# Kernel optimization log

Measured on AMD Instinct MI355X. Metric: run time of the kernel, lower is better.

Reference implementation:

```python
import jax, jax.numpy as jnp
import numpy as np

B, S, E, H = 2, 2048, 1024, 16
DH = E // H


def setup_inputs() -> dict:
    key = jax.random.key(0)
    ks = jax.random.split(key, 12)
    std = 1.0 / np.sqrt(E)
    inp = {
        "query": jax.random.normal(ks[0], (B, S, E), jnp.float32),
        "key": jax.random.normal(ks[1], (B, S, E), jnp.float32),
        "value": jax.random.normal(ks[2], (B, S, E), jnp.float32),
        "mask": jax.random.randint(ks[3], (B, 1, 1, S), 0, 2, jnp.int32),
        "Wq": jax.random.normal(ks[4], (E, E), jnp.float32) * std,
        "bq": jnp.zeros((E,), jnp.float32),
        "Wk": jax.random.normal(ks[5], (E, E), jnp.float32) * std,
        "bk": jnp.zeros((E,), jnp.float32),
        "Wv": jax.random.normal(ks[6], (E, E), jnp.float32) * std,
        "bv": jnp.zeros((E,), jnp.float32),
        "Wo": jax.random.normal(ks[7], (E, E), jnp.float32) * std,
        "bo": jnp.zeros((E,), jnp.float32),
    }
    return inp


def reference(query, key, value, mask, Wq, bq, Wk, bk, Wv, bv, Wo, bo):
    b = query.shape[0]
    # QKV projections, then split heads: [B,S,E] -> [B,H,S,Dh]
    def split_heads(x):
        return x.reshape(b, -1, H, DH).transpose(0, 2, 1, 3)
    q = split_heads(query @ Wq + bq)
    k = split_heads(key @ Wk + bk)
    v = split_heads(value @ Wv + bv)
    # explicit bmm -> mask -> softmax -> bmm (non-SDPA), scores [B,H,Sq,Sk]
    scores = jnp.einsum("bhqd,bhkd->bhqk", q, k) / np.sqrt(DH).astype(np.float32)
    scores = jnp.where(mask == 0, jnp.float32(-1e9), scores)
    attn = jax.nn.softmax(scores, axis=-1)  # dropout is identity in eval mode
    out = jnp.einsum("bhqk,bhkd->bhqd", attn, v)
    out = out.transpose(0, 2, 1, 3).reshape(b, -1, E)  # merge heads
    return out @ Wo + bo
```

## Files before the change

### kernel.cpp

```cpp
#include <hip/hip_runtime.h>
#include <hip/hip_bf16.h>
#include <stdint.h>

#define B_ 2
#define S_ 2048
#define E_ 1024
#define H_ 16
#define DH_ 64
#define MELEMS (4096 * 1024)
#define WE (1024 * 1024)

typedef unsigned short u16;
typedef __bf16 bf16x8 __attribute__((ext_vector_type(8)));
typedef u16 u16x8 __attribute__((ext_vector_type(8)));
typedef u16 u16x4 __attribute__((ext_vector_type(4)));
typedef float f32x4 __attribute__((ext_vector_type(4)));
typedef uint32_t u32x4 __attribute__((ext_vector_type(4)));

__device__ __forceinline__ float bf2f(u16 u) {
    union { uint32_t i; float f; } v; v.i = ((uint32_t)u) << 16; return v.f;
}
__device__ __forceinline__ u16 f2bf(float f) {
    union { float f; uint32_t i; } v; v.f = f;
    uint32_t r = (v.i + 0x7FFFu + ((v.i >> 16) & 1u)) >> 16;
    return (u16)r;
}
__device__ __forceinline__ uint32_t pkbf(float a, float b) {
    __hip_bfloat162 h = __float22bfloat162_rn(make_float2(a, b));
    uint32_t r; __builtin_memcpy(&r, &h, 4);
    return r;
}
__device__ __forceinline__ bf16x8 ldfrag(const u16* p) {
    u16x8 t = *(const u16x8*)p;
    return __builtin_bit_cast(bf16x8, t);
}
__device__ __forceinline__ void gld16(const void* g, void* l) {
    __builtin_amdgcn_global_load_lds(
        (const __attribute__((address_space(1))) void*)g,
        (__attribute__((address_space(3))) void*)l, 16, 0, 0);
}

__global__ __launch_bounds__(256)
void cvt_all(const float* __restrict__ q, const float* __restrict__ k,
             const float* __restrict__ v,
             const float* __restrict__ W0, const float* __restrict__ W1,
             const float* __restrict__ W2, const float* __restrict__ W3,
             u16* __restrict__ Qi, u16* __restrict__ Ki, u16* __restrict__ Vi,
             u16* __restrict__ T0, u16* __restrict__ T1,
             u16* __restrict__ T2, u16* __restrict__ T3)
{
    __shared__ float tile[64][65];
    const int bid = blockIdx.x;
    const int tid = threadIdx.x;

    if (bid < 6144) {
        const int z = bid >> 11;
        const int cx = bid & 2047;
        const float* src = (z == 0) ? q : (z == 1) ? k : v;
        u16* dst = (z == 0) ? Qi : (z == 1) ? Ki : Vi;
        const size_t i8 = ((size_t)cx * 256 + tid) * 8;
        float4 f0 = *(const float4*)&src[i8];
        float4 f1 = *(const float4*)&src[i8 + 4];
        u16x8 t;
        t[0] = f2bf(f0.x); t[1] = f2bf(f0.y); t[2] = f2bf(f0.z); t[3] = f2bf(f0.w);
        t[4] = f2bf(f1.x); t[5] = f2bf(f1.y); t[6] = f2bf(f1.z); t[7] = f2bf(f1.w);
        *(u16x8*)&dst[i8] = t;
    } else {
        const int rr = bid - 6144;
        const int z = rr >> 8;
        const int tt = rr & 255;
        const float* W = (z == 0) ? W0 : (z == 1) ? W1 : (z == 2) ? W2 : W3;
        u16* T = (z == 0) ? T0 : (z == 1) ? T1 : (z == 2) ? T2 : T3;
        const int n0 = (tt & 15) * 64, k0 = (tt >> 4) * 64;
        const int r = tid >> 2, c0 = (tid & 3) * 16;

        #pragma unroll
        for (int i = 0; i < 4; ++i) {
            float4 w = *(const float4*)&W[(size_t)(k0 + r) * 1024 + n0 + c0 + i * 4];
            tile[r][c0 + i * 4 + 0] = w.x; tile[r][c0 + i * 4 + 1] = w.y;
            tile[r][c0 + i * 4 + 2] = w.z; tile[r][c0 + i * 4 + 3] = w.w;
        }
        __syncthreads();
        u16x8 a, b;
        #pragma unroll
        for (int j = 0; j < 8; ++j) a[j] = f2bf(tile[c0 + j][r]);
        #pragma unroll
        for (int j = 0; j < 8; ++j) b[j] = f2bf(tile[c0 + 8 + j][r]);
        *(u16x8*)&T[(size_t)(n0 + r) * 1024 + k0 + c0] = a;
        *(u16x8*)&T[(size_t)(n0 + r) * 1024 + k0 + c0 + 8] = b;
    }
}

template<int BN>
__global__ __launch_bounds__(256)
void gemm_bt(const u16* __restrict__ A0, const u16* __restrict__ A1,
             const u16* __restrict__ A2,
             const u16* __restrict__ Bt0, const u16* __restrict__ Bt1,
             const u16* __restrict__ Bt2,
             const float* __restrict__ b0, const float* __restrict__ b1,
             const float* __restrict__ b2,
             void* __restrict__ C0, void* __restrict__ C1, void* __restrict__ C2,
             int c_f32, int vt_z, float scale0, int K)
{
    const int z = blockIdx.z;
    const u16* A  = (z == 0) ? A0 : (z == 1) ? A1 : A2;
    const u16* Bt = (z == 0) ? Bt0 : (z == 1) ? Bt1 : Bt2;
    const float* bias = (z == 0) ? b0 : (z == 1) ? b1 : b2;
    void* C = (z == 0) ? C0 : (z == 1) ? C1 : C2;
    const float scale = (z == 0) ? scale0 : 1.0f;

    __shared__ alignas(16) u16 As[128 * 32];
    __shared__ alignas(16) u16 Bs[BN * 32];

    const int tid  = threadIdx.x;
    const int lane = tid & 63;
    const int wv   = tid >> 6;
    const int l15  = lane & 15;
    const int quad = lane >> 4;
    const int m0 = blockIdx.y * 128;
    const int n0 = blockIdx.x * BN;
    const int wr = (wv >> 1) * 64;
    const int wc = (wv & 1) * (BN / 2);

    const int srow = wv * 16 + (lane >> 2);
    const int skk  = (lane & 3) * 8;

    constexpr int NJ = BN / 32;
    f32x4 acc[4][NJ] = {};

    for (int k0 = 0; k0 < K; k0 += 32) {
        __syncthreads();
        #pragma unroll
        for (int h = 0; h < 2; ++h) {
            const int r = h * 64 + srow;
            gld16(&A[(size_t)(m0 + r) * K + k0 + skk], &As[r * 32 + skk]);
        }
        #pragma unroll
        for (int h = 0; h < BN / 64; ++h) {
            const int r = h * 64 + srow;
            gld16(&Bt[(size_t)(n0 + r) * K + k0 + skk], &Bs[r * 32 + skk]);
        }
        __syncthreads();

        bf16x8 a[4], b[NJ];
        #pragma unroll
        for (int i = 0; i < 4; ++i)
            a[i] = ldfrag(&As[(wr + i * 16 + l15) * 32 + quad * 8]);
        #pragma unroll
        for (int j = 0; j < NJ; ++j)
            b[j] = ldfrag(&Bs[(wc + j * 16 + l15) * 32 + quad * 8]);
        #pragma unroll
        for (int i = 0; i < 4; ++i)
            #pragma unroll
            for (int j = 0; j < NJ; ++j)
                acc[i][j] = __builtin_amdgcn_mfma_f32_16x16x32_bf16(
                    a[i], b[j], acc[i][j], 0, 0, 0);
    }

    #pragma unroll
    for (int j = 0; j < NJ; ++j) {
        const int col = n0 + wc + j * 16 + l15;
        const float bcol = bias[col];
        #pragma unroll
        for (int i = 0; i < 4; ++i) {
            if (z == vt_z) {
                const int row0 = m0 + wr + i * 16 + quad * 4;
                const int bb = row0 >> 11, s0 = row0 & 2047;
                u16x4 t;
                #pragma unroll
                for (int r = 0; r < 4; ++r) t[r] = f2bf((acc[i][j][r] + bcol) * scale);
                *(u16x4*)&((u16*)C)[((size_t)bb * E_ + col) * S_ + s0] = t;
            } else {
                #pragma unroll
                for (int r = 0; r < 4; ++r) {
                    const int row = m0 + wr + i * 16 + quad * 4 + r;
                    const float v = (acc[i][j][r] + bcol) * scale;
                    if (c_f32) ((float*)C)[(size_t)row * 1024 + col] = v;
                    else       ((u16*)C)[(size_t)row * 1024 + col]  = f2bf(v);
                }
            }
        }
    }
}

__global__ __launch_bounds__(256, 2)
void attn_v5(const u16* __restrict__ Q, const u16* __restrict__ K,
             const u16* __restrict__ Vt_g, const int* __restrict__ mask,
             u16* __restrict__ ctx)
{
    __shared__ alignas(16) u16 Ks[2][64 * 64];
    __shared__ alignas(16) u16 Vs[2][64 * 64];
    __shared__ alignas(16) float Sb[4][32 * 68];

    const int tid  = threadIdx.x;
    const int lane = tid & 63;
    const int wv   = tid >> 6;
    const int l15  = lane & 15;
    const int quad = lane >> 4;
    const int sw   = l15 & 7;
    const int qt = blockIdx.x;
    const int bh = blockIdx.y;
    const int b  = bh >> 4, h = bh & 15;

    const size_t qk_off = (size_t)b * S_ * E_ + (size_t)h * DH_;
    const size_t vt_off = ((size_t)b * E_ + (size_t)h * DH_) * S_;

    const int qr0 = qt * 128 + wv * 16 + l15;
    const int qr1 = qr0 + 64;
    const bf16x8 qa0 = ldfrag(&Q[qk_off + (size_t)qr0 * E_ + quad * 8]);
    const bf16x8 qa1 = ldfrag(&Q[qk_off + (size_t)qr0 * E_ + 32 + quad * 8]);
    const bf16x8 qb0 = ldfrag(&Q[qk_off + (size_t)qr1 * E_ + quad * 8]);
    const bf16x8 qb1 = ldfrag(&Q[qk_off + (size_t)qr1 * E_ + 32 + quad * 8]);

    u16x8 ou;
    #pragma unroll
    for (int j = 0; j < 8; ++j) ou[j] = 0x3F80;
    const bf16x8 ones = __builtin_bit_cast(bf16x8, ou);

    f32x4 oacc[2][4] = {};
    f32x4 lacc[2] = {};

    const int srow = tid >> 3;
    const int sp   = tid & 7;
    const int sg   = sp ^ (srow & 7);

    auto stage = [&](int kc, int buf) {
        #pragma unroll
        for (int g = 0; g < 2; ++g) {
            const int r = g * 32 + srow;
            gld16(&K[qk_off + (size_t)(kc + r) * E_ + sg * 8],
                  &Ks[buf][r * 64 + sp * 8]);
            gld16(&Vt_g[vt_off + (size_t)r * S_ + kc + sg * 8],
                  &Vs[buf][r * 64 + sp * 8]);
        }
    };

    stage(0, 0);
    int cur = 0;

    for (int kc = 0; kc < S_; kc += 64) {
        __syncthreads();
        if (kc + 64 < S_) stage(kc + 64, cur ^ 1);

        #pragma unroll
        for (int t = 0; t < 4; ++t) {
            const int R = t * 16 + l15;
            bf16x8 kf0 = ldfrag(&Ks[cur][R * 64 + (quad ^ sw) * 8]);
            bf16x8 kf1 = ldfrag(&Ks[cur][R * 64 + ((4 + quad) ^ sw) * 8]);
            f32x4 s0 = {}, s1 = {};
            s0 = __builtin_amdgcn_mfma_f32_16x16x32_bf16(qa0, kf0, s0, 0, 0, 0);
            s0 = __builtin_amdgcn_mfma_f32_16x16x32_bf16(qa1, kf1, s0, 0, 0, 0);
            s1 = __builtin_amdgcn_mfma_f32_16x16x32_bf16(qb0, kf0, s1, 0, 0, 0);
            s1 = __builtin_amdgcn_mfma_f32_16x16x32_bf16(qb1, kf1, s1, 0, 0, 0);
            const int mv = mask[b * S_ + kc + t * 16 + l15];
            #pragma unroll
            for (int r = 0; r < 4; ++r) {
                Sb[wv][(quad * 4 + r) * 68 + t * 16 + l15]      = mv ? s0[r] : -1e9f;
                Sb[wv][(16 + quad * 4 + r) * 68 + t * 16 + l15] = mv ? s1[r] : -1e9f;
            }
        }

        bf16x8 pa[2][2];
        #pragma unroll
        for (int s = 0; s < 2; ++s) {
            const float* row = &Sb[wv][(s * 16 + l15) * 68];
            f32x4 s0a = *(const f32x4*)&row[quad * 8];
            f32x4 s0b = *(const f32x4*)&row[quad * 8 + 4];
            f32x4 s1a = *(const f32x4*)&row[32 + quad * 8];
            f32x4 s1b = *(const f32x4*)&row[32 + quad * 8 + 4];
            u32x4 w0, w1;
            w0[0] = pkbf(__expf(s0a[0]), __expf(s0a[1]));
            w0[1] = pkbf(__expf(s0a[2]), __expf(s0a[3]));
            w0[2] = pkbf(__expf(s0b[0]), __expf(s0b[1]));
            w0[3] = pkbf(__expf(s0b[2]), __expf(s0b[3]));
            w1[0] = pkbf(__expf(s1a[0]), __expf(s1a[1]));
            w1[1] = pkbf(__expf(s1a[2]), __expf(s1a[3]));
            w1[2] = pkbf(__expf(s1b[0]), __expf(s1b[1]));
            w1[3] = pkbf(__expf(s1b[2]), __expf(s1b[3]));
            pa[s][0] = __builtin_bit_cast(bf16x8, w0);
            pa[s][1] = __builtin_bit_cast(bf16x8, w1);
        }

        #pragma unroll
        for (int c = 0; c < 4; ++c) {
            const int D = c * 16 + l15;
            bf16x8 vb0 = ldfrag(&Vs[cur][D * 64 + (quad ^ sw) * 8]);
            bf16x8 vb1 = ldfrag(&Vs[cur][D * 64 + ((4 + quad) ^ sw) * 8]);
            #pragma unroll
            for (int s = 0; s < 2; ++s) {
                oacc[s][c] = __builtin_amdgcn_mfma_f32_16x16x32_bf16(pa[s][0], vb0, oacc[s][c], 0, 0, 0);
                oacc[s][c] = __builtin_amdgcn_mfma_f32_16x16x32_bf16(pa[s][1], vb1, oacc[s][c], 0, 0, 0);
            }
        }
        #pragma unroll
        for (int s = 0; s < 2; ++s) {
            lacc[s] = __builtin_amdgcn_mfma_f32_16x16x32_bf16(pa[s][0], ones, lacc[s], 0, 0, 0);
            lacc[s] = __builtin_amdgcn_mfma_f32_16x16x32_bf16(pa[s][1], ones, lacc[s], 0, 0, 0);
        }
        cur ^= 1;
    }

    #pragma unroll
    for (int s = 0; s < 2; ++s)
        #pragma unroll
        for (int c = 0; c < 4; ++c) {
            const int e = h * DH_ + c * 16 + l15;
            #pragma unroll
            for (int r = 0; r < 4; ++r) {
                const int qg = qt * 128 + s * 64 + wv * 16 + quad * 4 + r;
                ctx[((size_t)b * S_ + qg) * E_ + e] = f2bf(oacc[s][c][r] / lacc[s][r]);
            }
        }
}

__global__ __launch_bounds__(256)
void gemm_bias(const void* __restrict__ A, int a_f32,
               const float* __restrict__ W, const float* __restrict__ bias,
               void* __restrict__ C, int c_f32,
               int M, int N, int K, float scale)
{
    __shared__ alignas(16) u16 As[64 * 32];
    __shared__ alignas(16) u16 Wt[64 * 32];
    const int tid  = threadIdx.x;
    const int lane = tid & 63;
    const int wv   = tid >> 6;
    const int l15  = lane & 15;
    const int quad = lane >> 4;
    const int m0 = blockIdx.y * 64, n0 = blockIdx.x * 64;
    const int wr = (wv >> 1) * 32, wc = (wv & 1) * 32;
    const int ar = tid >> 2, ac = (tid & 3) * 8;
    const int wk = tid >> 3, wn = (tid & 7) * 8;
    f32x4 acc[2][2] = {};
    for (int k0 = 0; k0 < K; k0 += 32) {
        __syncthreads();
        if (a_f32) {
            const float* Af = (const float*)A;
            const float* p = &Af[(size_t)(m0 + ar) * K + k0 + ac];
            float4 f0 = *(const float4*)p; float4 f1 = *(const float4*)(p + 4);
            u16x8 t;
            t[0] = f2bf(f0.x); t[1] = f2bf(f0.y); t[2] = f2bf(f0.z); t[3] = f2bf(f0.w);
            t[4] = f2bf(f1.x); t[5] = f2bf(f1.y); t[6] = f2bf(f1.z); t[7] = f2bf(f1.w);
            *(u16x8*)&As[ar * 32 + ac] = t;
        } else {
            const u16* Ab = (const u16*)A;
            *(u16x8*)&As[ar * 32 + ac] = *(const u16x8*)&Ab[(size_t)(m0 + ar) * K + k0 + ac];
        }
        {
            const float* p = &W[(size_t)(k0 + wk) * N + n0 + wn];
            float4 g0 = *(const float4*)p; float4 g1 = *(const float4*)(p + 4);
            float fv[8] = {g0.x, g0.y, g0.z, g0.w, g1.x, g1.y, g1.z, g1.w};
            #pragma unroll
            for (int j = 0; j < 8; ++j) Wt[(wn + j) * 32 + wk] = f2bf(fv[j]);
        }
        __syncthreads();
        bf16x8 a[2], b[2];
        #pragma unroll
        for (int sm = 0; sm < 2; ++sm) a[sm] = ldfrag(&As[(wr + sm * 16 + l15) * 32 + quad * 8]);
        #pragma unroll
        for (int sn = 0; sn < 2; ++sn) b[sn] = ldfrag(&Wt[(wc + sn * 16 + l15) * 32 + quad * 8]);
        #pragma unroll
        for (int sm = 0; sm < 2; ++sm)
            #pragma unroll
            for (int sn = 0; sn < 2; ++sn)
                acc[sm][sn] = __builtin_amdgcn_mfma_f32_16x16x32_bf16(a[sm], b[sn], acc[sm][sn], 0, 0, 0);
    }
    #pragma unroll
    for (int sm = 0; sm < 2; ++sm)
        #pragma unroll
        for (int sn = 0; sn < 2; ++sn) {
            const int col = n0 + wc + sn * 16 + l15;
            const float bcol = bias[col];
            #pragma unroll
            for (int r = 0; r < 4; ++r) {
                const int row = m0 + wr + sm * 16 + quad * 4 + r;
                const float v = (acc[sm][sn][r] + bcol) * scale;
                if (c_f32) ((float*)C)[(size_t)row * N + col] = v;
                else       ((u16*)C)[(size_t)row * N + col]  = f2bf(v);
            }
        }
}

__global__ __launch_bounds__(256)
void attn_v2(const u16* __restrict__ Q, const u16* __restrict__ K,
             const u16* __restrict__ V, const int* __restrict__ mask,
             u16* __restrict__ ctx, int BH_per_B)
{
    __shared__ alignas(16) u16 Ks[64 * 72];
    __shared__ alignas(16) u16 Vt[64 * 72];
    __shared__ alignas(16) u16 Pb[4][16 * 72];
    const int tid  = threadIdx.x;
    const int lane = tid & 63;
    const int wv   = tid >> 6;
    const int l15  = lane & 15;
    const int quad = lane >> 4;
    const int qt = blockIdx.x;
    const int bh = blockIdx.y;
    const int b  = bh / BH_per_B, h = bh % BH_per_B;
    const size_t headoff = (size_t)b * S_ * E_ + (size_t)h * DH_;
    const int qrow = qt * 64 + wv * 16 + l15;
    const bf16x8 qf0 = ldfrag(&Q[headoff + (size_t)qrow * E_ + quad * 8]);
    const bf16x8 qf1 = ldfrag(&Q[headoff + (size_t)qrow * E_ + 32 + quad * 8]);
    f32x4 oacc[4] = {};
    float mrun[4] = {-1e30f, -1e30f, -1e30f, -1e30f};
    float lrun[4] = {0.f, 0.f, 0.f, 0.f};
    const int skey = tid >> 2;
    const int sd0  = (tid & 3) * 16;
    for (int kc = 0; kc < S_; kc += 64) {
        __syncthreads();
        {
            const u16* kg = &K[headoff + (size_t)(kc + skey) * E_ + sd0];
            *(u16x8*)&Ks[skey * 72 + sd0]     = *(const u16x8*)kg;
            *(u16x8*)&Ks[skey * 72 + sd0 + 8] = *(const u16x8*)(kg + 8);
            const u16* vg = &V[headoff + (size_t)(kc + skey) * E_ + sd0];
            u16x8 v0 = *(const u16x8*)vg;
            u16x8 v1 = *(const u16x8*)(vg + 8);
            #pragma unroll
            for (int j = 0; j < 8; ++j) {
                const int d = sd0 + j;
                Vt[d * 72 + (skey ^ (((d >> 3) & 7) * 8))] = v0[j];
            }
            #pragma unroll
            for (int j = 0; j < 8; ++j) {
                const int d = sd0 + 8 + j;
                Vt[d * 72 + (skey ^ (((d >> 3) & 7) * 8))] = v1[j];
            }
        }
        __syncthreads();
        f32x4 sb[4];
        #pragma unroll
        for (int t = 0; t < 4; ++t) {
            bf16x8 kf0 = ldfrag(&Ks[(t * 16 + l15) * 72 + quad * 8]);
            bf16x8 kf1 = ldfrag(&Ks[(t * 16 + l15) * 72 + 32 + quad * 8]);
            f32x4 s = {};
            s = __builtin_amdgcn_mfma_f32_16x16x32_bf16(qf0, kf0, s, 0, 0, 0);
            s = __builtin_amdgcn_mfma_f32_16x16x32_bf16(qf1, kf1, s, 0, 0, 0);
            const int mv = mask[b * S_ + kc + t * 16 + l15];
            #pragma unroll
            for (int r = 0; r < 4; ++r) sb[t][r] = (mv == 0) ? -1e9f : s[r];
        }
        #pragma unroll
        for (int r = 0; r < 4; ++r) {
            float m = fmaxf(fmaxf(sb[0][r], sb[1][r]), fmaxf(sb[2][r], sb[3][r]));
            #pragma unroll
            for (int off = 1; off < 16; off <<= 1) m = fmaxf(m, __shfl_xor(m, off));
            const float mnew  = fmaxf(mrun[r], m);
            const float alpha = __expf(mrun[r] - mnew);
            mrun[r] = mnew;
            float sum = 0.f;
            #pragma unroll
            for (int t = 0; t < 4; ++t) {
                const float p = __expf(sb[t][r] - mnew);
                sb[t][r] = p; sum += p;
            }
            #pragma unroll
            for (int off = 1; off < 16; off <<= 1) sum += __shfl_xor(sum, off);
            lrun[r] = lrun[r] * alpha + sum;
            #pragma unroll
            for (int c = 0; c < 4; ++c) oacc[c][r] *= alpha;
        }
        #pragma unroll
        for (int t = 0; t < 4; ++t)
            #pragma unroll
            for (int r = 0; r < 4; ++r)
                Pb[wv][(quad * 4 + r) * 72 + t * 16 + l15] = f2bf(sb[t][r]);
        const bf16x8 pa0 = ldfrag(&Pb[wv][l15 * 72 + quad * 8]);
        const bf16x8 pa1 = ldfrag(&Pb[wv][l15 * 72 + 32 + quad * 8]);
        #pragma unroll
        for (int c = 0; c < 4; ++c) {
            const int d = c * 16 + l15;
            const int sg = ((d >> 3) & 7) * 8;
            bf16x8 vb0 = ldfrag(&Vt[d * 72 + ((quad * 8) ^ sg)]);
            bf16x8 vb1 = ldfrag(&Vt[d * 72 + ((32 + quad * 8) ^ sg)]);
            oacc[c] = __builtin_amdgcn_mfma_f32_16x16x32_bf16(pa0, vb0, oacc[c], 0, 0, 0);
            oacc[c] = __builtin_amdgcn_mfma_f32_16x16x32_bf16(pa1, vb1, oacc[c], 0, 0, 0);
        }
    }
    #pragma unroll
    for (int c = 0; c < 4; ++c) {
        const int e = h * DH_ + c * 16 + l15;
        #pragma unroll
        for (int r = 0; r < 4; ++r) {
            const int qg = qt * 64 + wv * 16 + quad * 4 + r;
            ctx[((size_t)b * S_ + qg) * E_ + e] = f2bf(oacc[c][r] / lrun[r]);
        }
    }
}

extern "C" void kernel_launch(void* const* d_in, const int* in_sizes, int n_in,
                              void* d_out, int out_size, void* d_ws, size_t ws_size,
                              hipStream_t stream)
{
    const float* query = (const float*)d_in[0];
    const float* key   = (const float*)d_in[1];
    const float* value = (const float*)d_in[2];
    const int*   mask  = (const int*)d_in[3];
    const float* Wq = (const float*)d_in[4];  const float* bq = (const float*)d_in[5];
    const float* Wk = (const float*)d_in[6];  const float* bk = (const float*)d_in[7];
    const float* Wv = (const float*)d_in[8];  const float* bv = (const float*)d_in[9];
    const float* Wo = (const float*)d_in[10]; const float* bo = (const float*)d_in[11];
    float* out = (float*)d_out;

    u16* ws = (u16*)d_ws;
    dim3 blk(256);

    const size_t need_fancy = (size_t)(6 * MELEMS + 4 * WE) * sizeof(u16);
    const size_t need_full  = (size_t)(4 * MELEMS) * sizeof(u16) + 64;

    if (ws_size >= need_fancy) {
        u16* Qi  = ws;
        u16* Ki  = Qi + MELEMS;
        u16* Vi  = Ki + MELEMS;
        u16* Wqt = Vi + MELEMS;
        u16* Wkt = Wqt + WE;
        u16* Wvt = Wkt + WE;
        u16* Wot = Wvt + WE;
        u16* Qp  = Wot + WE;
        u16* Kp  = Qp + MELEMS;
        u16* Vp  = Kp + MELEMS;
        u16* Cp  = Qi;

        cvt_all<<<dim3(7168), blk, 0, stream>>>(query, key, value,
                                                Wq, Wk, Wv, Wo,
                                                Qi, Ki, Vi, Wqt, Wkt, Wvt, Wot);

        gemm_bt<128><<<dim3(8, 32, 3), blk, 0, stream>>>(
            Qi, Ki, Vi, Wqt, Wkt, Wvt, bq, bk, bv,
            Qp, Kp, Vp, 0, 2, 0.125f, E_);

        attn_v5<<<dim3(S_ / 128, B_ * H_), blk, 0, stream>>>(Qp, Kp, Vp, mask, Cp);

        gemm_bt<64><<<dim3(16, 32, 1), blk, 0, stream>>>(
            Cp, Cp, Cp, Wot, Wot, Wot, bo, bo, bo,
            out, out, out, 1, -1, 1.0f, E_);
    } else if (ws_size >= need_full) {
        u16* Qp = ws;
        u16* Kp = ws + MELEMS;
        u16* Vp = ws + 2 * MELEMS;
        u16* Cp = ws + 3 * MELEMS;
        const int M = B_ * S_;
        dim3 gg(E_ / 64, M / 64);
        gemm_bias<<<gg, blk, 0, stream>>>(query, 1, Wq, bq, Qp, 0, M, E_, E_, 0.125f);
        gemm_bias<<<gg, blk, 0, stream>>>(key,   1, Wk, bk, Kp, 0, M, E_, E_, 1.0f);
        gemm_bias<<<gg, blk, 0, stream>>>(value, 1, Wv, bv, Vp, 0, M, E_, E_, 1.0f);
        attn_v2<<<dim3(S_ / 64, B_ * H_), blk, 0, stream>>>(Qp, Kp, Vp, mask, Cp, H_);
        gemm_bias<<<gg, blk, 0, stream>>>(Cp, 0, Wo, bo, out, 1, M, E_, E_, 1.0f);
    } else {
        const size_t szb = (size_t)S_ * E_;
        u16* Qp = ws; u16* Kp = ws + szb; u16* Vp = ws + 2 * szb; u16* Cp = ws + 3 * szb;
        dim3 gg(E_ / 64, S_ / 64);
        for (int b = 0; b < B_; ++b) {
            gemm_bias<<<gg, blk, 0, stream>>>(query + b * szb, 1, Wq, bq, Qp, 0, S_, E_, E_, 0.125f);
            gemm_bias<<<gg, blk, 0, stream>>>(key   + b * szb, 1, Wk, bk, Kp, 0, S_, E_, E_, 1.0f);
            gemm_bias<<<gg, blk, 0, stream>>>(value + b * szb, 1, Wv, bv, Vp, 0, S_, E_, E_, 1.0f);
            attn_v2<<<dim3(S_ / 64, H_), blk, 0, stream>>>(Qp, Kp, Vp, mask + b * S_, Cp, H_);
            gemm_bias<<<gg, blk, 0, stream>>>(Cp, 0, Wo, bo, ((float*)d_out) + b * szb, 1, S_, E_, E_, 1.0f);
        }
    }
}
```

Before: 153.3 us.

## Keep attention scores in registers via transposed MFMA and permlane16 swap

Removes the per-wave LDS score buffer. Q·K^T is computed transposed so each lane holds the scores for its own key columns, and the P fragments are then regrouped with permlane16_swap instead of a round trip through shared memory. The V fragment read order is permuted to match. Masking is applied by zeroing the exponential with vectorized int4 mask loads, and log2(e) is folded into the Q projection scale so exp2 replaces expf. The smaller LDS footprint allows launch bounds of 3 blocks per CU, at a risk of register pressure.

```diff
diff --git a/kernel.cpp b/kernel.cpp
--- a/kernel.cpp
+++ b/kernel.cpp
@@ -16,6 +16,7 @@
 typedef u16 u16x4 __attribute__((ext_vector_type(4)));
 typedef float f32x4 __attribute__((ext_vector_type(4)));
 typedef uint32_t u32x4 __attribute__((ext_vector_type(4)));
+typedef uint32_t u32x2v __attribute__((ext_vector_type(2)));
 
 __device__ __forceinline__ float bf2f(u16 u) {
     union { uint32_t i; float f; } v; v.i = ((uint32_t)u) << 16; return v.f;
@@ -183,14 +184,13 @@
     }
 }
 
-__global__ __launch_bounds__(256, 2)
-void attn_v5(const u16* __restrict__ Q, const u16* __restrict__ K,
+__global__ __launch_bounds__(256, 3)
+void attn_v6(const u16* __restrict__ Q, const u16* __restrict__ K,
              const u16* __restrict__ Vt_g, const int* __restrict__ mask,
              u16* __restrict__ ctx)
 {
     __shared__ alignas(16) u16 Ks[2][64 * 64];
     __shared__ alignas(16) u16 Vs[2][64 * 64];
-    __shared__ alignas(16) float Sb[4][32 * 68];
 
     const int tid  = threadIdx.x;
     const int lane = tid & 63;
@@ -198,6 +198,7 @@
     const int l15  = lane & 15;
     const int quad = lane >> 4;
     const int sw   = l15 & 7;
+    const int kq   = (quad & 1) * 2 + (quad >> 1);
     const int qt = blockIdx.x;
     const int bh = blockIdx.y;
     const int b  = bh >> 4, h = bh & 15;
@@ -238,54 +239,59 @@
     stage(0, 0);
     int cur = 0;
 
+    const int* mrow = &mask[b * S_];
+
     for (int kc = 0; kc < S_; kc += 64) {
         __syncthreads();
         if (kc + 64 < S_) stage(kc + 64, cur ^ 1);
 
-        #pragma unroll
-        for (int t = 0; t < 4; ++t) {
-            const int R = t * 16 + l15;
-            bf16x8 kf0 = ldfrag(&Ks[cur][R * 64 + (quad ^ sw) * 8]);
-            bf16x8 kf1 = ldfrag(&Ks[cur][R * 64 + ((4 + quad) ^ sw) * 8]);
-            f32x4 s0 = {}, s1 = {};
-            s0 = __builtin_amdgcn_mfma_f32_16x16x32_bf16(qa0, kf0, s0, 0, 0, 0);
-            s0 = __builtin_amdgcn_mfma_f32_16x16x32_bf16(qa1, kf1, s0, 0, 0, 0);
-            s1 = __builtin_amdgcn_mfma_f32_16x16x32_bf16(qb0, kf0, s1, 0, 0, 0);
-            s1 = __builtin_amdgcn_mfma_f32_16x16x32_bf16(qb1, kf1, s1, 0, 0, 0);
-            const int mv = mask[b * S_ + kc + t * 16 + l15];
-            #pragma unroll
-            for (int r = 0; r < 4; ++r) {
-                Sb[wv][(quad * 4 + r) * 68 + t * 16 + l15]      = mv ? s0[r] : -1e9f;
-                Sb[wv][(16 + quad * 4 + r) * 68 + t * 16 + l15] = mv ? s1[r] : -1e9f;
-            }
-        }
-
         bf16x8 pa[2][2];
         #pragma unroll
-        for (int s = 0; s < 2; ++s) {
-            const float* row = &Sb[wv][(s * 16 + l15) * 68];
-            f32x4 s0a = *(const f32x4*)&row[quad * 8];
-            f32x4 s0b = *(const f32x4*)&row[quad * 8 + 4];
-            f32x4 s1a = *(const f32x4*)&row[32 + quad * 8];
-            f32x4 s1b = *(const f32x4*)&row[32 + quad * 8 + 4];
-            u32x4 w0, w1;
-            w0[0] = pkbf(__expf(s0a[0]), __expf(s0a[1]));
-            w0[1] = pkbf(__expf(s0a[2]), __expf(s0a[3]));
-            w0[2] = pkbf(__expf(s0b[0]), __expf(s0b[1]));
-            w0[3] = pkbf(__expf(s0b[2]), __expf(s0b[3]));
-            w1[0] = pkbf(__expf(s1a[0]), __expf(s1a[1]));
-            w1[1] = pkbf(__expf(s1a[2]), __expf(s1a[3]));
-            w1[2] = pkbf(__expf(s1b[0]), __expf(s1b[1]));
-            w1[3] = pkbf(__expf(s1b[2]), __expf(s1b[3]));
-            pa[s][0] = __builtin_bit_cast(bf16x8, w0);
-            pa[s][1] = __builtin_bit_cast(bf16x8, w1);
+        for (int hh = 0; hh < 2; ++hh) {
+            f32x4 st[2][2];
+            #pragma unroll
+            for (int tt = 0; tt < 2; ++tt) {
+                const int R = (hh * 2 + tt) * 16 + l15;
+                bf16x8 kf0 = ldfrag(&Ks[cur][R * 64 + (quad ^ sw) * 8]);
+                bf16x8 kf1 = ldfrag(&Ks[cur][R * 64 + ((4 + quad) ^ sw) * 8]);
+                f32x4 s0 = {}, s1 = {};
+                s0 = __builtin_amdgcn_mfma_f32_16x16x32_bf16(kf0, qa0, s0, 0, 0, 0);
+                s0 = __builtin_amdgcn_mfma_f32_16x16x32_bf16(kf1, qa1, s0, 0, 0, 0);
+                s1 = __builtin_amdgcn_mfma_f32_16x16x32_bf16(kf0, qb0, s1, 0, 0, 0);
+                s1 = __builtin_amdgcn_mfma_f32_16x16x32_bf16(kf1, qb1, s1, 0, 0, 0);
+                st[tt][0] = s0; st[tt][1] = s1;
+            }
+            const int kb = kc + hh * 32 + quad * 4;
+            const int4 m0 = *(const int4*)&mrow[kb];
+            const int4 m1 = *(const int4*)&mrow[kb + 16];
+            #pragma unroll
+            for (int s = 0; s < 2; ++s) {
+                const f32x4 p0 = st[0][s], p1 = st[1][s];
+                const float e00 = m0.x ? __builtin_exp2f(p0[0]) : 0.f;
+                const float e01 = m0.y ? __builtin_exp2f(p0[1]) : 0.f;
+                const float e02 = m0.z ? __builtin_exp2f(p0[2]) : 0.f;
+                const float e03 = m0.w ? __builtin_exp2f(p0[3]) : 0.f;
+                const float e10 = m1.x ? __builtin_exp2f(p1[0]) : 0.f;
+                const float e11 = m1.y ? __builtin_exp2f(p1[1]) : 0.f;
+                const float e12 = m1.z ? __builtin_exp2f(p1[2]) : 0.f;
+                const float e13 = m1.w ? __builtin_exp2f(p1[3]) : 0.f;
+                const uint32_t wA = pkbf(e00, e01);
+                const uint32_t wB = pkbf(e02, e03);
+                const uint32_t wC = pkbf(e10, e11);
+                const uint32_t wD = pkbf(e12, e13);
+                u32x2v rAC = __builtin_amdgcn_permlane16_swap(wA, wC, false, false);
+                u32x2v rBD = __builtin_amdgcn_permlane16_swap(wB, wD, false, false);
+                u32x4 w;
+                w[0] = rAC[0]; w[1] = rBD[0]; w[2] = rAC[1]; w[3] = rBD[1];
+                pa[s][hh] = __builtin_bit_cast(bf16x8, w);
+            }
         }
 
         #pragma unroll
         for (int c = 0; c < 4; ++c) {
-            const int D = c * 16 + l15;
-            bf16x8 vb0 = ldfrag(&Vs[cur][D * 64 + (quad ^ sw) * 8]);
-            bf16x8 vb1 = ldfrag(&Vs[cur][D * 64 + ((4 + quad) ^ sw) * 8]);
+            const int Dd = c * 16 + l15;
+            bf16x8 vb0 = ldfrag(&Vs[cur][Dd * 64 + ((0 + kq) ^ sw) * 8]);
+            bf16x8 vb1 = ldfrag(&Vs[cur][Dd * 64 + ((4 + kq) ^ sw) * 8]);
             #pragma unroll
             for (int s = 0; s < 2; ++s) {
                 oacc[s][c] = __builtin_amdgcn_mfma_f32_16x16x32_bf16(pa[s][0], vb0, oacc[s][c], 0, 0, 0);
@@ -525,9 +531,9 @@
 
         gemm_bt<128><<<dim3(8, 32, 3), blk, 0, stream>>>(
             Qi, Ki, Vi, Wqt, Wkt, Wvt, bq, bk, bv,
-            Qp, Kp, Vp, 0, 2, 0.125f, E_);
-
-        attn_v5<<<dim3(S_ / 128, B_ * H_), blk, 0, stream>>>(Qp, Kp, Vp, mask, Cp);
+            Qp, Kp, Vp, 0, 2, 0.125f * 1.44269504f, E_);
+
+        attn_v6<<<dim3(S_ / 128, B_ * H_), blk, 0, stream>>>(Qp, Kp, Vp, mask, Cp);
 
         gemm_bt<64><<<dim3(16, 32, 1), blk, 0, stream>>>(
             Cp, Cp, Cp, Wot, Wot, Wot, bo, bo, bo,
```

New measurement: 173.0 us. 12.8% more time.
